# Kernel tuning notes

Hardware: AMD Instinct MI355X
Metric: run time of the kernel (lower is better)

The kernel has to match this reference:

```python
import jax, jax.numpy as jnp
import numpy as np

D_IN = 1024
D_OUT = 1024
SEQ = 4096


def setup_inputs() -> dict:
    key = jax.random.key(0)
    kx, kq, kk, kv = jax.random.split(key, 4)
    x = jax.random.normal(kx, (SEQ, D_IN), dtype=jnp.float32)
    # torch Linear weights: [d_out, d_in], y = x @ W.T; no bias (qkv_bias=False)
    s = 1.0 / np.sqrt(D_IN)
    Wq = jax.random.uniform(kq, (D_OUT, D_IN), dtype=jnp.float32, minval=-s, maxval=s)
    Wk = jax.random.uniform(kk, (D_OUT, D_IN), dtype=jnp.float32, minval=-s, maxval=s)
    Wv = jax.random.uniform(kv, (D_OUT, D_IN), dtype=jnp.float32, minval=-s, maxval=s)
    return {"x": x, "Wq": Wq, "Wk": Wk, "Wv": Wv}


def reference(x, Wq, Wk, Wv):
    seq = x.shape[0]
    q = x @ Wq.T  # [S, d_out]
    k = x @ Wk.T
    v = x @ Wv.T
    scores = q @ k.T  # [S, S]
    # causal mask: positions j > i masked to -inf (triu, diagonal=1)
    causal = jnp.tril(jnp.ones((seq, seq), dtype=bool))
    scores = jnp.where(causal, scores, -jnp.inf)
    attn = jax.nn.softmax(scores / jnp.sqrt(jnp.float32(q.shape[-1])), axis=-1)
    return attn @ v  # [S, d_out]
```

## Files before the change

### kernel.cpp

```cpp
#include <hip/hip_runtime.h>
#include <hip/hip_bf16.h>
#include <cstdint>
#include <cstddef>


#define SEQQ 4096
#define DDIM 1024

typedef __bf16 bf16x8 __attribute__((ext_vector_type(8)));
typedef float f32x4 __attribute__((ext_vector_type(4)));

__device__ __forceinline__ unsigned short f2bf(float f) {
  unsigned int u = __builtin_bit_cast(unsigned int, f);
  unsigned int r = u + 0x7FFFu + ((u >> 16) & 1u);
  return (unsigned short)(r >> 16);
}

__device__ __forceinline__ void gload_lds16(const void* g, void* lds) {
  __builtin_amdgcn_global_load_lds(
      (__attribute__((address_space(1))) void*)(uintptr_t)g,
      (__attribute__((address_space(3))) void*)(uintptr_t)lds, 16, 0, 0);
}

__global__ __launch_bounds__(256) void cvt_all(const float* __restrict__ x,
                                               const float* __restrict__ Wq,
                                               const float* __restrict__ Wk,
                                               const float* __restrict__ Wv,
                                               unsigned short* __restrict__ xb,
                                               unsigned short* __restrict__ Wcat) {
  int b = blockIdx.x;
  const float* src;
  unsigned short* dst;
  float scale = 1.0f;
  if (b < 4096) {
    src = x; dst = xb;
  } else if (b < 5120) {
    src = Wq; dst = Wcat; scale = 0.03125f; b -= 4096;
  } else if (b < 6144) {
    src = Wk; dst = Wcat + (1u << 20); b -= 5120;
  } else {
    src = Wv; dst = Wcat + (2u << 20); b -= 6144;
  }
  const int i = (b * 256 + threadIdx.x) * 4;
  const float4 v = *reinterpret_cast<const float4*>(src + i);
  ushort4 o;
  o.x = f2bf(v.x * scale);
  o.y = f2bf(v.y * scale);
  o.z = f2bf(v.z * scale);
  o.w = f2bf(v.w * scale);
  *reinterpret_cast<ushort4*>(dst + i) = o;
}

#define GEMM_PRE()                                                          \
  __shared__ unsigned short As[3][8192] __attribute__((aligned(16)));       \
  __shared__ unsigned short Bs[3][8192] __attribute__((aligned(16)));       \
  const int tid = threadIdx.x;                                              \
  const int wave = tid >> 6, lane = tid & 63;                               \
  const int wr = (wave >> 2) * 128, wc = (wave & 3) * 64;                   \
  f32x4 acc[8][4] = {};                                                     \
  int offA[8], offB[4];                                                     \
  {                                                                         \
    const int cb = (lane >> 4) * 16;                                        \
    const int rA = wr + (lane & 15);                                        \
    _Pragma("unroll")                                                       \
    for (int m = 0; m < 8; ++m) {                                           \
      int o = (rA + m * 16) * 64 + cb;                                      \
      offA[m] = o ^ (((o >> 9) & 1) << 5);                                  \
    }                                                                       \
    const int rB = wc + (lane & 15);                                        \
    _Pragma("unroll")                                                       \
    for (int n = 0; n < 4; ++n) {                                           \
      int o = (rB + n * 16) * 64 + cb;                                      \
      offB[n] = o ^ (((o >> 9) & 1) << 5);                                  \
    }                                                                       \
  }

#define GEMM_LOOP(ABASE, LDA, BBASE, LDB, S0, S1)                           \
  do {                                                                      \
    const int nt = (S1) - (S0);                                             \
    const char *pA0, *pA1, *pB0, *pB1;                                      \
    {                                                                       \
      const size_t srow = wave * 16 + (lane >> 2);                          \
      const int scb = ((lane & 3) * 16) ^ (((lane >> 5) & 1) << 5);         \
      pA0 = (const char*)(ABASE) + srow * ((size_t)(LDA) * 2) +             \
            (size_t)(S0) * 64 + scb;                                        \
      pA1 = pA0 + (size_t)128 * ((size_t)(LDA) * 2);                        \
      pB0 = (const char*)(BBASE) + srow * ((size_t)(LDB) * 2) +             \
            (size_t)(S0) * 64 + scb;                                        \
      pB1 = pB0 + (size_t)128 * ((size_t)(LDB) * 2);                        \
    }                                                                       \
    char* ldsA = (char*)&As[0][0];                                          \
    char* ldsB = (char*)&Bs[0][0];                                          \
    const int wofs = wave * 1024;                                           \
    gload_lds16(pA0, ldsA + wofs);                                          \
    gload_lds16(pA1, ldsA + 8192 + wofs);                                   \
    gload_lds16(pB0, ldsB + wofs);                                          \
    gload_lds16(pB1, ldsB + 8192 + wofs);                                   \
    pA0 += 64; pA1 += 64; pB0 += 64; pB1 += 64;                             \
    if (nt > 1) {                                                           \
      gload_lds16(pA0, ldsA + 16384 + wofs);                                \
      gload_lds16(pA1, ldsA + 16384 + 8192 + wofs);                         \
      gload_lds16(pB0, ldsB + 16384 + wofs);                                \
      gload_lds16(pB1, ldsB + 16384 + 8192 + wofs);                         \
      pA0 += 64; pA1 += 64; pB0 += 64; pB1 += 64;                           \
      asm volatile("s_waitcnt vmcnt(4)" ::: "memory");                      \
    } else {                                                                \
      asm volatile("s_waitcnt vmcnt(0)" ::: "memory");                      \
    }                                                                       \
    asm volatile("s_barrier" ::: "memory");                                 \
    int rb = 0;                                                             \
    for (int s = 0; s < nt; ++s) {                                          \
      const int bofs = rb * 16384;                                          \
      bf16x8 a[8], b[4];                                                    \
      _Pragma("unroll")                                                     \
      for (int m = 0; m < 8; ++m)                                           \
        a[m] = *(const bf16x8*)(ldsA + bofs + offA[m]);                     \
      _Pragma("unroll")                                                     \
      for (int n = 0; n < 4; ++n)                                           \
        b[n] = *(const bf16x8*)(ldsB + bofs + offB[n]);                     \
      if (s + 2 < nt) {                                                     \
        const int wofs2 = ((rb >= 1) ? rb - 1 : 2) * 16384 + wofs;          \
        gload_lds16(pA0, ldsA + wofs2);                                     \
        gload_lds16(pA1, ldsA + wofs2 + 8192);                              \
        gload_lds16(pB0, ldsB + wofs2);                                     \
        gload_lds16(pB1, ldsB + wofs2 + 8192);                              \
        pA0 += 64; pA1 += 64; pB0 += 64; pB1 += 64;                         \
        asm volatile("s_waitcnt lgkmcnt(0)" ::: "memory");                  \
        asm volatile("s_waitcnt vmcnt(4)" ::: "memory");                    \
      } else if (s + 1 < nt) {                                              \
        asm volatile("s_waitcnt lgkmcnt(0)" ::: "memory");                  \
        asm volatile("s_waitcnt vmcnt(0)" ::: "memory");                    \
      } else {                                                              \
        asm volatile("s_waitcnt lgkmcnt(0)" ::: "memory");                  \
      }                                                                     \
      asm volatile("s_barrier" ::: "memory");                               \
      __builtin_amdgcn_s_setprio(1);                                        \
      _Pragma("unroll")                                                     \
      for (int m = 0; m < 8; ++m)                                           \
        _Pragma("unroll")                                                   \
        for (int n = 0; n < 4; ++n)                                         \
          acc[m][n] = __builtin_amdgcn_mfma_f32_16x16x32_bf16(              \
              a[m], b[n], acc[m][n], 0, 0, 0);                              \
      __builtin_amdgcn_s_setprio(0);                                        \
      rb = (rb == 2) ? 0 : rb + 1;                                          \
    }                                                                       \
  } while (0)

__global__ __launch_bounds__(512, 1) void gemm_qkv(const unsigned short* __restrict__ X,
                                                   const unsigned short* __restrict__ W,
                                                   unsigned short* __restrict__ Qb,
                                                   unsigned short* __restrict__ Kb,
                                                   unsigned short* __restrict__ Vt) {
  GEMM_PRE();
  const int brow = blockIdx.y * 256, bcol = blockIdx.x * 256;
  GEMM_LOOP(X + (size_t)brow * DDIM, DDIM, W + (size_t)bcol * DDIM, DDIM, 0, 32);
  const int region = bcol >> 10;
  const int lcol = bcol & 1023;
  const int c0 = wc + (lane & 15);
  const int r0 = wr + ((lane >> 4) << 2);
  if (region < 2) {
    unsigned short* dst = (region == 0) ? Qb : Kb;
#pragma unroll
    for (int m = 0; m < 8; ++m) {
      const int r = brow + r0 + m * 16;
#pragma unroll
      for (int n = 0; n < 4; ++n) {
        const int c = lcol + c0 + n * 16;
#pragma unroll
        for (int j = 0; j < 4; ++j)
          dst[(size_t)(r + j) * DDIM + c] = f2bf(acc[m][n][j]);
      }
    }
  } else {
#pragma unroll
    for (int m = 0; m < 8; ++m) {
      const int r = brow + r0 + m * 16;
#pragma unroll
      for (int n = 0; n < 4; ++n) {
        const int c = lcol + c0 + n * 16;
        ushort4 pk;
        pk.x = f2bf(acc[m][n][0]);
        pk.y = f2bf(acc[m][n][1]);
        pk.z = f2bf(acc[m][n][2]);
        pk.w = f2bf(acc[m][n][3]);
        *reinterpret_cast<ushort4*>(Vt + (size_t)c * SEQQ + r) = pk;
      }
    }
  }
}

__global__ __launch_bounds__(512, 1) void gemm_qkt(const unsigned short* __restrict__ Qb,
                                                   const unsigned short* __restrict__ Kb,
                                                   unsigned short* __restrict__ S) {
  const int bi = blockIdx.y, bj = blockIdx.x;
  if (bj > bi) return;
  GEMM_PRE();
  const int brow = bi * 256, bcol = bj * 256;
  GEMM_LOOP(Qb + (size_t)brow * DDIM, DDIM, Kb + (size_t)bcol * DDIM, DDIM, 0, 32);
  const int c0 = wc + (lane & 15);
  const int r0 = wr + ((lane >> 4) << 2);
#pragma unroll
  for (int m = 0; m < 8; ++m) {
    const int r = brow + r0 + m * 16;
#pragma unroll
    for (int n = 0; n < 4; ++n) {
      const int c = bcol + c0 + n * 16;
#pragma unroll
      for (int j = 0; j < 4; ++j) {
        unsigned short o = (c > r + j) ? (unsigned short)0xFF80
                                       : f2bf(acc[m][n][j]);
        S[(size_t)(r + j) * SEQQ + c] = o;
      }
    }
  }
}

__global__ __launch_bounds__(256) void softmax_causal(unsigned short* __restrict__ S) {
  const int row = blockIdx.x;
  const int L = ((row >> 8) + 1) << 8;
  unsigned short* Srow = S + (size_t)row * SEQQ;
  __shared__ float red[4];
  const int tid = threadIdx.x;
  const int lane = tid & 63, wave = tid >> 6;

  float x[16];
  bool have[2];
  float m = -3.0e38f;
#pragma unroll
  for (int it = 0; it < 2; ++it) {
    const int j = tid * 8 + it * 2048;
    have[it] = (j < L);
    if (have[it]) {
      const uint4 v = *reinterpret_cast<const uint4*>(Srow + j);
      const unsigned u[4] = {v.x, v.y, v.z, v.w};
#pragma unroll
      for (int q = 0; q < 4; ++q) {
        x[it * 8 + q * 2] = __builtin_bit_cast(float, u[q] << 16);
        x[it * 8 + q * 2 + 1] = __builtin_bit_cast(float, u[q] & 0xFFFF0000u);
      }
#pragma unroll
      for (int q = 0; q < 8; ++q) m = fmaxf(m, x[it * 8 + q]);
    }
  }
#pragma unroll
  for (int o = 32; o; o >>= 1) m = fmaxf(m, __shfl_xor(m, o));
  if (lane == 0) red[wave] = m;
  __syncthreads();
  m = fmaxf(fmaxf(red[0], red[1]), fmaxf(red[2], red[3]));
  __syncthreads();

  float sum = 0.f;
#pragma unroll
  for (int it = 0; it < 2; ++it)
    if (have[it]) {
#pragma unroll
      for (int q = 0; q < 8; ++q) {
        x[it * 8 + q] = __expf(x[it * 8 + q] - m);
        sum += x[it * 8 + q];
      }
    }
#pragma unroll
  for (int o = 32; o; o >>= 1) sum += __shfl_xor(sum, o);
  if (lane == 0) red[wave] = sum;
  __syncthreads();
  sum = red[0] + red[1] + red[2] + red[3];
  const float inv = 1.0f / sum;

#pragma unroll
  for (int it = 0; it < 2; ++it)
    if (have[it]) {
      const int j = tid * 8 + it * 2048;
      unsigned u[4];
#pragma unroll
      for (int q = 0; q < 4; ++q) {
        u[q] = (unsigned)f2bf(x[it * 8 + q * 2] * inv) |
               ((unsigned)f2bf(x[it * 8 + q * 2 + 1] * inv) << 16);
      }
      *reinterpret_cast<uint4*>(Srow + j) = make_uint4(u[0], u[1], u[2], u[3]);
    }
}

__device__ __forceinline__ int pv_nc(int bi) { return (bi >> 2) + 1; }
__device__ __forceinline__ int pv_rcbase(int bi) {
  const int g = bi >> 2, r = bi & 3;
  return 2 * g * (g - 1) + r * g;
}

__global__ __launch_bounds__(512, 1) void gemm_pv_split(const unsigned short* __restrict__ P,
                                                        const unsigned short* __restrict__ Vt,
                                                        float* __restrict__ O,
                                                        float* __restrict__ part) {
  const int bj = blockIdx.x, bi = blockIdx.y, ck = blockIdx.z;
  const int nc = pv_nc(bi);
  if (ck >= nc) return;
  const int kt = (bi + 1) * 8;
  const int W = (kt + nc - 1) / nc;
  const int s0 = ck * W;
  const int s1 = min(s0 + W, kt);
  if (s0 >= s1) return;

  GEMM_PRE();
  const int brow = bi * 256, bcol = bj * 256;
  GEMM_LOOP(P + (size_t)brow * SEQQ, SEQQ, Vt + (size_t)bcol * SEQQ, SEQQ, s0, s1);
  const int c0 = wc + (lane & 15);
  const int r0 = wr + ((lane >> 4) << 2);
  if (ck == 0) {
#pragma unroll
    for (int m = 0; m < 8; ++m) {
      const int r = brow + r0 + m * 16;
#pragma unroll
      for (int n = 0; n < 4; ++n) {
        const int c = bcol + c0 + n * 16;
#pragma unroll
        for (int j = 0; j < 4; ++j)
          O[(size_t)(r + j) * DDIM + c] = acc[m][n][j];
      }
    }
  } else {
    float* tile = part + ((size_t)(pv_rcbase(bi) + (ck - 1)) * 4 + bj) * 65536;
#pragma unroll
    for (int m = 0; m < 8; ++m) {
      const int lr = r0 + m * 16;
#pragma unroll
      for (int n = 0; n < 4; ++n) {
        const int lc = c0 + n * 16;
#pragma unroll
        for (int j = 0; j < 4; ++j)
          tile[(lr + j) * 256 + lc] = acc[m][n][j];
      }
    }
  }
}

__global__ __launch_bounds__(256) void reduce_pv(float* __restrict__ O,
                                                 const float* __restrict__ part) {
  const int idx = blockIdx.x * 256 + threadIdx.x;
  const int r = 1024 + (idx >> 8);
  const int cc = (idx & 255) * 4;
  const int bi = r >> 8;
  const int nparts = bi >> 2;
  const int rcb = pv_rcbase(bi);
  const int bj = cc >> 8;
  const int lr = r & 255, lc = cc & 255;
  float4 acc = *reinterpret_cast<float4*>(O + (size_t)r * DDIM + cc);
  for (int k = 0; k < nparts; ++k) {
    const float4 p = *reinterpret_cast<const float4*>(
        part + ((size_t)(rcb + k) * 4 + bj) * 65536 + lr * 256 + lc);
    acc.x += p.x; acc.y += p.y; acc.z += p.z; acc.w += p.w;
  }
  *reinterpret_cast<float4*>(O + (size_t)r * DDIM + cc) = acc;
}

extern "C" void kernel_launch(void* const* d_in, const int* in_sizes, int n_in,
                              void* d_out, int out_size, void* d_ws, size_t ws_size,
                              hipStream_t stream) {
  (void)in_sizes; (void)n_in; (void)out_size; (void)ws_size;
  const float* x = (const float*)d_in[0];
  const float* Wq = (const float*)d_in[1];
  const float* Wk = (const float*)d_in[2];
  const float* Wv = (const float*)d_in[3];
  float* out = (float*)d_out;

  char* ws = (char*)d_ws;
  unsigned short* xb   = (unsigned short*)(ws);
  unsigned short* Wcat = (unsigned short*)(ws + ((size_t)8 << 20));
  unsigned short* Qb   = (unsigned short*)(ws + ((size_t)14 << 20));
  unsigned short* Kb   = (unsigned short*)(ws + ((size_t)22 << 20));
  unsigned short* Vt   = (unsigned short*)(ws + ((size_t)30 << 20));
  unsigned short* S    = (unsigned short*)(ws + ((size_t)38 << 20));
  float* part = (float*)ws;

  cvt_all<<<7168, 256, 0, stream>>>(x, Wq, Wk, Wv, xb, Wcat);
  gemm_qkv<<<dim3(12, 16), 512, 0, stream>>>(xb, Wcat, Qb, Kb, Vt);
  gemm_qkt<<<dim3(16, 16), 512, 0, stream>>>(Qb, Kb, S);
  softmax_causal<<<SEQQ, 256, 0, stream>>>(S);
  gemm_pv_split<<<dim3(4, 16, 4), 512, 0, stream>>>(S, Vt, out, part);
  reduce_pv<<<3072, 256, 0, stream>>>(out, part);
}
```

Baseline: 127.5 us.

## Double-buffer LDS fragments in registers to overlap reads with MFMA

Restructures the GEMM main loop so the A/B fragments for the next K-tile are read from LDS into a second register set right after the barrier, before the current tile's MFMAs are issued. The loop is unrolled by two to alternate between the even and odd register sets, and scheduling barriers keep the wait counters ordered. The aim is to hide LDS read latency behind matrix instructions instead of stalling before each MFMA block. In exchange it uses roughly 48 more VGPRs per thread, which raises register pressure in a kernel limited to one block per CU.

```diff
diff --git a/kernel.cpp b/kernel.cpp
--- a/kernel.cpp
+++ b/kernel.cpp
@@ -75,6 +75,49 @@
     }                                                                       \
   }
 
+#define GEMM_STEP(AC, BC, AN, BN, s)                                        \
+  {                                                                         \
+    if ((s) + 2 < nt) {                                                     \
+      const int wb = (rb >= 1) ? rb - 1 : 2;                                \
+      const int wofs2 = wb * 16384 + wofs;                                  \
+      gload_lds16(pA0, ldsA + wofs2);                                       \
+      gload_lds16(pA1, ldsA + wofs2 + 8192);                                \
+      gload_lds16(pB0, ldsB + wofs2);                                       \
+      gload_lds16(pB1, ldsB + wofs2 + 8192);                                \
+      pA0 += 64; pA1 += 64; pB0 += 64; pB1 += 64;                           \
+      asm volatile("s_waitcnt lgkmcnt(0)" ::: "memory");                    \
+      __builtin_amdgcn_sched_barrier(0);                                    \
+      asm volatile("s_waitcnt vmcnt(4)" ::: "memory");                      \
+    } else if ((s) + 1 < nt) {                                              \
+      asm volatile("s_waitcnt lgkmcnt(0)" ::: "memory");                    \
+      __builtin_amdgcn_sched_barrier(0);                                    \
+      asm volatile("s_waitcnt vmcnt(0)" ::: "memory");                      \
+    } else {                                                                \
+      asm volatile("s_waitcnt lgkmcnt(0)" ::: "memory");                    \
+      __builtin_amdgcn_sched_barrier(0);                                    \
+    }                                                                       \
+    asm volatile("s_barrier" ::: "memory");                                 \
+    if ((s) + 1 < nt) {                                                     \
+      const int rbn = (rb == 2) ? 0 : rb + 1;                               \
+      const int nofs = rbn * 16384;                                         \
+      _Pragma("unroll")                                                     \
+      for (int m = 0; m < 8; ++m)                                           \
+        AN[m] = *(const bf16x8*)(ldsA + nofs + offA[m]);                    \
+      _Pragma("unroll")                                                     \
+      for (int n = 0; n < 4; ++n)                                           \
+        BN[n] = *(const bf16x8*)(ldsB + nofs + offB[n]);                    \
+    }                                                                       \
+    __builtin_amdgcn_s_setprio(1);                                          \
+    _Pragma("unroll")                                                       \
+    for (int m = 0; m < 8; ++m)                                             \
+      _Pragma("unroll")                                                     \
+      for (int n = 0; n < 4; ++n)                                           \
+        acc[m][n] = __builtin_amdgcn_mfma_f32_16x16x32_bf16(                \
+            AC[m], BC[n], acc[m][n], 0, 0, 0);                              \
+    __builtin_amdgcn_s_setprio(0);                                          \
+    rb = (rb == 2) ? 0 : rb + 1;                                            \
+  }
+
 #define GEMM_LOOP(ABASE, LDA, BBASE, LDB, S0, S1)                           \
   do {                                                                      \
     const int nt = (S1) - (S0);                                             \
@@ -108,42 +151,18 @@
       asm volatile("s_waitcnt vmcnt(0)" ::: "memory");                      \
     }                                                                       \
     asm volatile("s_barrier" ::: "memory");                                 \
+    bf16x8 aE[8], bE[4], aO[8], bO[4];                                      \
+    _Pragma("unroll")                                                       \
+    for (int m = 0; m < 8; ++m) aE[m] = *(const bf16x8*)(ldsA + offA[m]);   \
+    _Pragma("unroll")                                                       \
+    for (int n = 0; n < 4; ++n) bE[n] = *(const bf16x8*)(ldsB + offB[n]);   \
     int rb = 0;                                                             \
-    for (int s = 0; s < nt; ++s) {                                          \
-      const int bofs = rb * 16384;                                          \
-      bf16x8 a[8], b[4];                                                    \
-      _Pragma("unroll")                                                     \
-      for (int m = 0; m < 8; ++m)                                           \
-        a[m] = *(const bf16x8*)(ldsA + bofs + offA[m]);                     \
-      _Pragma("unroll")                                                     \
-      for (int n = 0; n < 4; ++n)                                           \
-        b[n] = *(const bf16x8*)(ldsB + bofs + offB[n]);                     \
-      if (s + 2 < nt) {                                                     \
-        const int wofs2 = ((rb >= 1) ? rb - 1 : 2) * 16384 + wofs;          \
-        gload_lds16(pA0, ldsA + wofs2);                                     \
-        gload_lds16(pA1, ldsA + wofs2 + 8192);                              \
-        gload_lds16(pB0, ldsB + wofs2);                                     \
-        gload_lds16(pB1, ldsB + wofs2 + 8192);                              \
-        pA0 += 64; pA1 += 64; pB0 += 64; pB1 += 64;                         \
-        asm volatile("s_waitcnt lgkmcnt(0)" ::: "memory");                  \
-        asm volatile("s_waitcnt vmcnt(4)" ::: "memory");                    \
-      } else if (s + 1 < nt) {                                              \
-        asm volatile("s_waitcnt lgkmcnt(0)" ::: "memory");                  \
-        asm volatile("s_waitcnt vmcnt(0)" ::: "memory");                    \
-      } else {                                                              \
-        asm volatile("s_waitcnt lgkmcnt(0)" ::: "memory");                  \
-      }                                                                     \
-      asm volatile("s_barrier" ::: "memory");                               \
-      __builtin_amdgcn_s_setprio(1);                                        \
-      _Pragma("unroll")                                                     \
-      for (int m = 0; m < 8; ++m)                                           \
-        _Pragma("unroll")                                                   \
-        for (int n = 0; n < 4; ++n)                                         \
-          acc[m][n] = __builtin_amdgcn_mfma_f32_16x16x32_bf16(              \
-              a[m], b[n], acc[m][n], 0, 0, 0);                              \
-      __builtin_amdgcn_s_setprio(0);                                        \
-      rb = (rb == 2) ? 0 : rb + 1;                                          \
-    }                                                                       \
+    int s = 0;                                                              \
+    for (; s + 1 < nt; s += 2) {                                            \
+      GEMM_STEP(aE, bE, aO, bO, s);                                         \
+      GEMM_STEP(aO, bO, aE, bE, s + 1);                                     \
+    }                                                                       \
+    if (s < nt) GEMM_STEP(aE, bE, aO, bO, s);                               \
   } while (0)
 
 __global__ __launch_bounds__(512, 1) void gemm_qkv(const unsigned short* __restrict__ X,
```

Measured after the change: 131.3 us. 3.0% more time.

## Switch GEMM mainloop to double-buffered 64-wide K stages with split MFMA halves

Applied to the files above, without the earlier changes.

The shared GEMM mainloop goes from a three-deep ring of 32-wide K tiles to a two-deep ring of 64-wide K tiles. Each stage loads two 32-column halves and interleaves their LDS reads with two MFMA batches, so there is half as many barriers and vmcnt waits per unit of K. Loop trip counts in all three GEMM kernels are halved to match. The trade-off is shallower prefetch: a full vmcnt(0) wait every iteration, with only one stage in flight instead of two, and LDS use grows from 96KB to 128KB per block.

```diff
diff --git a/kernel.cpp b/kernel.cpp
--- a/kernel.cpp
+++ b/kernel.cpp
@@ -52,8 +52,8 @@
 }
 
 #define GEMM_PRE()                                                          \
-  __shared__ unsigned short As[3][8192] __attribute__((aligned(16)));       \
-  __shared__ unsigned short Bs[3][8192] __attribute__((aligned(16)));       \
+  __shared__ unsigned short As[2][32768 / 2] __attribute__((aligned(16)));  \
+  __shared__ unsigned short Bs[2][32768 / 2] __attribute__((aligned(16)));  \
   const int tid = threadIdx.x;                                              \
   const int wave = tid >> 6, lane = tid & 63;                               \
   const int wr = (wave >> 2) * 128, wc = (wave & 3) * 64;                   \
@@ -75,42 +75,44 @@
     }                                                                       \
   }
 
+#define STAGE(BOFS)                                                         \
+  {                                                                         \
+    gload_lds16(sA00, ldsA + (BOFS) + dC0);                                 \
+    gload_lds16(sA01, ldsA + (BOFS) + dC1);                                 \
+    gload_lds16(sA10, ldsA + (BOFS) + 16384 + dC0);                         \
+    gload_lds16(sA11, ldsA + (BOFS) + 16384 + dC1);                         \
+    gload_lds16(sB00, ldsB + (BOFS) + dC0);                                 \
+    gload_lds16(sB01, ldsB + (BOFS) + dC1);                                 \
+    gload_lds16(sB10, ldsB + (BOFS) + 16384 + dC0);                         \
+    gload_lds16(sB11, ldsB + (BOFS) + 16384 + dC1);                         \
+    sA00 += 128; sA01 += 128; sA10 += 128; sA11 += 128;                     \
+    sB00 += 128; sB01 += 128; sB10 += 128; sB11 += 128;                     \
+  }
+
 #define GEMM_LOOP(ABASE, LDA, BBASE, LDB, S0, S1)                           \
   do {                                                                      \
     const int nt = (S1) - (S0);                                             \
-    const char *pA0, *pA1, *pB0, *pB1;                                      \
-    {                                                                       \
-      const size_t srow = wave * 16 + (lane >> 2);                          \
-      const int scb = ((lane & 3) * 16) ^ (((lane >> 5) & 1) << 5);         \
-      pA0 = (const char*)(ABASE) + srow * ((size_t)(LDA) * 2) +             \
-            (size_t)(S0) * 64 + scb;                                        \
-      pA1 = pA0 + (size_t)128 * ((size_t)(LDA) * 2);                        \
-      pB0 = (const char*)(BBASE) + srow * ((size_t)(LDB) * 2) +             \
-            (size_t)(S0) * 64 + scb;                                        \
-      pB1 = pB0 + (size_t)128 * ((size_t)(LDB) * 2);                        \
-    }                                                                       \
+    const size_t lda2 = (size_t)(LDA) * 2, ldb2 = (size_t)(LDB) * 2;        \
+    const int r0s = wave * 16 + (lane >> 2);                                \
+    const int scb = ((lane & 3) * 16) ^ (((lane >> 5) & 1) << 5);           \
+    const char* sA00 = (const char*)(ABASE) + (size_t)r0s * lda2 +          \
+                       (size_t)(S0) * 128 + scb;                            \
+    const char* sA01 = sA00 + 128 * lda2;                                   \
+    const char* sA10 = sA00 + 64;                                           \
+    const char* sA11 = sA01 + 64;                                           \
+    const char* sB00 = (const char*)(BBASE) + (size_t)r0s * ldb2 +          \
+                       (size_t)(S0) * 128 + scb;                            \
+    const char* sB01 = sB00 + 128 * ldb2;                                   \
+    const char* sB10 = sB00 + 64;                                           \
+    const char* sB11 = sB01 + 64;                                           \
     char* ldsA = (char*)&As[0][0];                                          \
     char* ldsB = (char*)&Bs[0][0];                                          \
-    const int wofs = wave * 1024;                                           \
-    gload_lds16(pA0, ldsA + wofs);                                          \
-    gload_lds16(pA1, ldsA + 8192 + wofs);                                   \
-    gload_lds16(pB0, ldsB + wofs);                                          \
-    gload_lds16(pB1, ldsB + 8192 + wofs);                                   \
-    pA0 += 64; pA1 += 64; pB0 += 64; pB1 += 64;                             \
-    if (nt > 1) {                                                           \
-      gload_lds16(pA0, ldsA + 16384 + wofs);                                \
-      gload_lds16(pA1, ldsA + 16384 + 8192 + wofs);                         \
-      gload_lds16(pB0, ldsB + 16384 + wofs);                                \
-      gload_lds16(pB1, ldsB + 16384 + 8192 + wofs);                         \
-      pA0 += 64; pA1 += 64; pB0 += 64; pB1 += 64;                           \
-      asm volatile("s_waitcnt vmcnt(4)" ::: "memory");                      \
-    } else {                                                                \
-      asm volatile("s_waitcnt vmcnt(0)" ::: "memory");                      \
-    }                                                                       \
+    const int dC0 = wave * 1024, dC1 = (8 + wave) * 1024;                   \
+    STAGE(0);                                                               \
+    asm volatile("s_waitcnt vmcnt(0)" ::: "memory");                        \
     asm volatile("s_barrier" ::: "memory");                                 \
-    int rb = 0;                                                             \
     for (int s = 0; s < nt; ++s) {                                          \
-      const int bofs = rb * 16384;                                          \
+      const int bofs = (s & 1) * 32768;                                     \
       bf16x8 a[8], b[4];                                                    \
       _Pragma("unroll")                                                     \
       for (int m = 0; m < 8; ++m)                                           \
@@ -118,22 +120,9 @@
       _Pragma("unroll")                                                     \
       for (int n = 0; n < 4; ++n)                                           \
         b[n] = *(const bf16x8*)(ldsB + bofs + offB[n]);                     \
-      if (s + 2 < nt) {                                                     \
-        const int wofs2 = ((rb >= 1) ? rb - 1 : 2) * 16384 + wofs;          \
-        gload_lds16(pA0, ldsA + wofs2);                                     \
-        gload_lds16(pA1, ldsA + wofs2 + 8192);                              \
-        gload_lds16(pB0, ldsB + wofs2);                                     \
-        gload_lds16(pB1, ldsB + wofs2 + 8192);                              \
-        pA0 += 64; pA1 += 64; pB0 += 64; pB1 += 64;                         \
-        asm volatile("s_waitcnt lgkmcnt(0)" ::: "memory");                  \
-        asm volatile("s_waitcnt vmcnt(4)" ::: "memory");                    \
-      } else if (s + 1 < nt) {                                              \
-        asm volatile("s_waitcnt lgkmcnt(0)" ::: "memory");                  \
-        asm volatile("s_waitcnt vmcnt(0)" ::: "memory");                    \
-      } else {                                                              \
-        asm volatile("s_waitcnt lgkmcnt(0)" ::: "memory");                  \
-      }                                                                     \
-      asm volatile("s_barrier" ::: "memory");                               \
+      if (s + 1 < nt) STAGE((~s & 1) * 32768);                              \
+      asm volatile("s_waitcnt lgkmcnt(0)" ::: "memory");                    \
+      __builtin_amdgcn_sched_barrier(0);                                    \
       __builtin_amdgcn_s_setprio(1);                                        \
       _Pragma("unroll")                                                     \
       for (int m = 0; m < 8; ++m)                                           \
@@ -142,7 +131,27 @@
           acc[m][n] = __builtin_amdgcn_mfma_f32_16x16x32_bf16(              \
               a[m], b[n], acc[m][n], 0, 0, 0);                              \
       __builtin_amdgcn_s_setprio(0);                                        \
-      rb = (rb == 2) ? 0 : rb + 1;                                          \
+      bf16x8 a2[8], b2[4];                                                  \
+      _Pragma("unroll")                                                     \
+      for (int m = 0; m < 8; ++m)                                           \
+        a2[m] = *(const bf16x8*)(ldsA + bofs + 16384 + offA[m]);            \
+      _Pragma("unroll")                                                     \
+      for (int n = 0; n < 4; ++n)                                           \
+        b2[n] = *(const bf16x8*)(ldsB + bofs + 16384 + offB[n]);            \
+      asm volatile("s_waitcnt lgkmcnt(0)" ::: "memory");                    \
+      __builtin_amdgcn_sched_barrier(0);                                    \
+      __builtin_amdgcn_s_setprio(1);                                        \
+      _Pragma("unroll")                                                     \
+      for (int m = 0; m < 8; ++m)                                           \
+        _Pragma("unroll")                                                   \
+        for (int n = 0; n < 4; ++n)                                         \
+          acc[m][n] = __builtin_amdgcn_mfma_f32_16x16x32_bf16(              \
+              a2[m], b2[n], acc[m][n], 0, 0, 0);                            \
+      __builtin_amdgcn_s_setprio(0);                                        \
+      if (s + 1 < nt) {                                                     \
+        asm volatile("s_waitcnt vmcnt(0)" ::: "memory");                    \
+        asm volatile("s_barrier" ::: "memory");                             \
+      }                                                                     \
     }                                                                       \
   } while (0)
 
@@ -153,7 +162,7 @@
                                                    unsigned short* __restrict__ Vt) {
   GEMM_PRE();
   const int brow = blockIdx.y * 256, bcol = blockIdx.x * 256;
-  GEMM_LOOP(X + (size_t)brow * DDIM, DDIM, W + (size_t)bcol * DDIM, DDIM, 0, 32);
+  GEMM_LOOP(X + (size_t)brow * DDIM, DDIM, W + (size_t)bcol * DDIM, DDIM, 0, 16);
   const int region = bcol >> 10;
   const int lcol = bcol & 1023;
   const int c0 = wc + (lane & 15);
@@ -196,7 +205,7 @@
   if (bj > bi) return;
   GEMM_PRE();
   const int brow = bi * 256, bcol = bj * 256;
-  GEMM_LOOP(Qb + (size_t)brow * DDIM, DDIM, Kb + (size_t)bcol * DDIM, DDIM, 0, 32);
+  GEMM_LOOP(Qb + (size_t)brow * DDIM, DDIM, Kb + (size_t)bcol * DDIM, DDIM, 0, 16);
   const int c0 = wc + (lane & 15);
   const int r0 = wr + ((lane >> 4) << 2);
 #pragma unroll
@@ -293,7 +302,7 @@
   const int bj = blockIdx.x, bi = blockIdx.y, ck = blockIdx.z;
   const int nc = pv_nc(bi);
   if (ck >= nc) return;
-  const int kt = (bi + 1) * 8;
+  const int kt = (bi + 1) * 4;
   const int W = (kt + nc - 1) / nc;
   const int s0 = ck * W;
   const int s1 = min(s0 + W, kt);
```

New measurement: 130.6 us. 2.4% more time.
